# Optimization experiments

Measured on AMD Instinct MI355X. Metric: run time of the kernel, lower is better.

The kernel has to match this reference:

```python
import jax, jax.numpy as jnp
import numpy as np

B, T, H = 64, 512, 256
D = 2 * H            # input dim to slot LSTM (bidirectional encoder repr)
MAX_SLOTS = 64       # max slot spans kept per sentence
MAX_LEN = 8          # max tokens per span
N_SLOT_TYPES = 64


def _pack_spans(bio):
    """Segment BIO tags into spans: each span = B token + following I tokens.
    Returns token index table [B, MAX_SLOTS, MAX_LEN] and validity mask."""
    bsz, t = bio.shape
    bmask = bio == 1
    imask = bio == 2
    sid = jnp.cumsum(bmask.astype(jnp.int32), axis=1) - 1      # span id per token
    valid = (bmask | imask) & (sid >= 0)
    cs = jnp.cumsum(valid.astype(jnp.int32), axis=1)           # running count of span tokens
    bi = jnp.arange(bsz)[:, None]
    # cs value at each span's B token (overflow spans dumped into slot MAX_SLOTS)
    sid_b = jnp.where(bmask & (sid < MAX_SLOTS), sid, MAX_SLOTS)
    start = jnp.zeros((bsz, MAX_SLOTS + 1), jnp.int32).at[bi, sid_b].set(cs)[:, :MAX_SLOTS]
    sid_c = jnp.clip(sid, 0, MAX_SLOTS - 1)
    rank = cs - jnp.take_along_axis(start, sid_c, axis=1)      # position within span (B token -> 0)
    ok = valid & (sid < MAX_SLOTS) & (rank < MAX_LEN)
    s_idx = jnp.where(ok, sid_c, MAX_SLOTS)
    r_idx = jnp.where(ok, rank, MAX_LEN)
    tpos = jnp.broadcast_to(jnp.arange(t, dtype=jnp.int32), (bsz, t))
    tok = jnp.zeros((bsz, MAX_SLOTS + 1, MAX_LEN + 1), jnp.int32).at[bi, s_idx, r_idx].set(tpos)
    vm = jnp.zeros((bsz, MAX_SLOTS + 1, MAX_LEN + 1), bool).at[bi, s_idx, r_idx].set(True)
    return tok[:, :MAX_SLOTS, :MAX_LEN], vm[:, :MAX_SLOTS, :MAX_LEN]


def _lstm(x, Wih, Whh, b):
    """Unidirectional LSTM. x: [N, L, D] -> outputs [N, L, H] (torch gate order i,f,g,o)."""
    xg = jnp.einsum('nld,gd->nlg', x, Wih) + b                 # [N, L, 4H]
    n, l, _ = xg.shape
    h0 = jnp.zeros((n, Whh.shape[1]), x.dtype)

    def step(carry, xt):
        h, c = carry
        g = xt + h @ Whh.T
        i, f, gg, o = jnp.split(g, 4, axis=-1)
        c = jax.nn.sigmoid(f) * c + jax.nn.sigmoid(i) * jnp.tanh(gg)
        h = jax.nn.sigmoid(o) * jnp.tanh(c)
        return (h, c), h

    _, hs = jax.lax.scan(step, (h0, h0), jnp.swapaxes(xg, 0, 1))
    return jnp.swapaxes(hs, 0, 1)


def reference(lstm_repr, W_ih_f, W_hh_f, b_f, W_ih_b, W_hh_b, b_b, slot_emb, bio):
    tok, vm = _pack_spans(bio)                                  # [B,MS,ML], [B,MS,ML]
    bi = jnp.arange(lstm_repr.shape[0])[:, None, None]
    spans = lstm_repr[bi, tok]                                  # [B,MS,ML,D]
    lens = vm.sum(-1)                                           # [B,MS]
    # reverse each span within its valid length (padding stays at the end)
    pos = jnp.arange(MAX_LEN)
    rpos = lens[..., None] - 1 - pos
    ridx = jnp.where(rpos >= 0, rpos, 0)
    spans_rev = jnp.take_along_axis(spans, ridx[..., None], axis=2)
    ms = MAX_SLOTS
    xf = spans.reshape(-1, MAX_LEN, D)
    xb = spans_rev.reshape(-1, MAX_LEN, D)
    m = vm.reshape(-1, MAX_LEN, 1).astype(lstm_repr.dtype)
    hf = _lstm(xf, W_ih_f, W_hh_f, b_f)                         # [B*MS, ML, H]
    hb = _lstm(xb, W_ih_b, W_hh_b, b_b)
    pooled = jnp.concatenate([(hf * m).sum(1), (hb * m).sum(1)], axis=-1)  # sum-pool over span
    pooled = pooled.reshape(lstm_repr.shape[0], ms, 2 * H)
    scores = jnp.einsum('bsh,kh->bsk', pooled, slot_emb)        # [B,MS,n_slot_types]
    scores = scores * (lens > 0)[..., None]
    return scores


def setup_inputs() -> dict:
    key = jax.random.key(0)
    ks = jax.random.split(key, 9)
    s = 0.05
    return {
        'lstm_repr': jax.random.normal(ks[0], (B, T, D), jnp.float32),
        'W_ih_f': jax.random.normal(ks[1], (4 * H, D), jnp.float32) * s,
        'W_hh_f': jax.random.normal(ks[2], (4 * H, H), jnp.float32) * s,
        'b_f': jax.random.normal(ks[3], (4 * H,), jnp.float32) * s,
        'W_ih_b': jax.random.normal(ks[4], (4 * H, D), jnp.float32) * s,
        'W_hh_b': jax.random.normal(ks[5], (4 * H, H), jnp.float32) * s,
        'b_b': jax.random.normal(ks[6], (4 * H,), jnp.float32) * s,
        'slot_emb': jax.random.normal(ks[7], (N_SLOT_TYPES, 2 * H), jnp.float32) * s,
        'bio': jax.random.randint(ks[8], (B, T), 0, 3, dtype=jnp.int32),
    }
```

## Files before the change

### kernel.cpp

```cpp
#include <hip/hip_runtime.h>
#include <hip/hip_bf16.h>
#include <stdint.h>

#define B_ 64
#define T_ 512
#define H_ 256
#define D_ 512
#define MS_ 64
#define ML_ 8
#define NST_ 64

typedef unsigned short u16;
typedef __bf16 bf8 __attribute__((ext_vector_type(8)));
typedef float f4 __attribute__((ext_vector_type(4)));

__device__ __forceinline__ u16 f2bf(float f) {
    unsigned u = __builtin_bit_cast(unsigned, f);
    u += 0x7fffu + ((u >> 16) & 1u);
    return (u16)(u >> 16);
}
__device__ __forceinline__ float bf2f(u16 v) {
    return __builtin_bit_cast(float, (unsigned)v << 16);
}
__device__ __forceinline__ float sigm(float x) { return 1.f / (1.f + __expf(-x)); }

__global__ __launch_bounds__(256) void build_wc2(const float* __restrict__ wihf,
                                                 const float* __restrict__ whhf,
                                                 const float* __restrict__ wihb,
                                                 const float* __restrict__ whhb,
                                                 const float* __restrict__ bf,
                                                 const float* __restrict__ bb,
                                                 u16* __restrict__ wcx,
                                                 u16* __restrict__ wch,
                                                 float* __restrict__ bc) {
    int i = blockIdx.x * 256 + threadIdx.x;
    if (i < 2 * 1024 * 768) {
        int dir = i / (1024 * 768);
        int rem = i - dir * 1024 * 768;
        int n = rem / 768;
        int k = rem - n * 768;
        int nn = n & 63, c = n >> 6;
        int orig = (nn >> 4) * 256 + c * 16 + (nn & 15);
        if (k < 512) {
            const float* wih = dir ? wihb : wihf;
            wcx[((size_t)dir * 1024 + n) * 512 + k] = f2bf(wih[orig * 512 + k]);
        } else {
            const float* whh = dir ? whhb : whhf;
            wch[((size_t)dir * 1024 + n) * 256 + (k - 512)] = f2bf(whh[orig * 256 + (k - 512)]);
        }
    } else if (i < 2 * 1024 * 768 + 2048) {
        int i2 = i - 2 * 1024 * 768;
        int dir = i2 >> 10;
        int n = i2 & 1023;
        int nn = n & 63, c = n >> 6;
        int orig = (nn >> 4) * 256 + c * 16 + (nn & 15);
        bc[i2] = (dir ? bb : bf)[orig];
    }
}

__global__ __launch_bounds__(256) void zero_ws(uint4* __restrict__ dst, int n4) {
    int i = blockIdx.x * 256 + threadIdx.x;
    if (i < n4) { uint4 z = {0u, 0u, 0u, 0u}; dst[i] = z; }
}

__global__ __launch_bounds__(512) void pack_spans2(const int* __restrict__ bio,
                                                   int* __restrict__ tok,
                                                   int* __restrict__ lenb) {
    __shared__ int wsum[8];
    __shared__ int start_s[64];
    __shared__ int len_s[64];
    int b = blockIdx.x;
    int t = threadIdx.x;
    int lane = t & 63, w = t >> 6;
    int v = bio[b * T_ + t];
    int bm = (v == 1);
    int im = (v == 2);
    if (t < 64) len_s[t] = 0;

    int x = bm;
#pragma unroll
    for (int off = 1; off < 64; off <<= 1) {
        int y = __shfl_up(x, off, 64);
        if (lane >= off) x += y;
    }
    if (lane == 63) wsum[w] = x;
    __syncthreads();
    int wof = 0;
    for (int i = 0; i < w; ++i) wof += wsum[i];
    int sid = x + wof - 1;
    int valid = ((bm | im) && sid >= 0) ? 1 : 0;
    __syncthreads();

    x = valid;
#pragma unroll
    for (int off = 1; off < 64; off <<= 1) {
        int y = __shfl_up(x, off, 64);
        if (lane >= off) x += y;
    }
    if (lane == 63) wsum[w] = x;
    __syncthreads();
    wof = 0;
    for (int i = 0; i < w; ++i) wof += wsum[i];
    int cs = x + wof;

    if (bm && sid < MS_) start_s[sid] = cs;
    __syncthreads();

    if (valid && sid < MS_) {
        int rank = cs - start_s[sid];
        if (rank < ML_) {
            tok[(b * MS_ + sid) * ML_ + rank] = t;
            atomicAdd(&len_s[sid], 1);
        }
    }
    __syncthreads();
    if (t < 64) lenb[b * MS_ + t] = len_s[t];
}

__global__ __launch_bounds__(256) void build_lists(const int* __restrict__ lenb,
                                                   int* __restrict__ lists,
                                                   int* __restrict__ counts) {
    __shared__ int wsum[4];
    int tid = threadIdx.x;
    int lane = tid & 63, w = tid >> 6;
    int len[16];
#pragma unroll
    for (int i = 0; i < 16; ++i) len[i] = lenb[tid * 16 + i];
    for (int p = 0; p < ML_; ++p) {
        int c = 0;
#pragma unroll
        for (int i = 0; i < 16; ++i) c += (len[i] > p) ? 1 : 0;
        int x = c;
#pragma unroll
        for (int off = 1; off < 64; off <<= 1) {
            int y = __shfl_up(x, off, 64);
            if (lane >= off) x += y;
        }
        if (lane == 63) wsum[w] = x;
        __syncthreads();
        int wof = 0;
        for (int i = 0; i < w; ++i) wof += wsum[i];
        int pos = wof + x - c;
#pragma unroll
        for (int i = 0; i < 16; ++i)
            if (len[i] > p) lists[p * 4096 + pos++] = tid * 16 + i;
        if (tid == 255) counts[p] = pos;
        __syncthreads();
    }
}

__global__ __launch_bounds__(64) void conv_gather(const float* __restrict__ repr,
                                                  const int* __restrict__ tok,
                                                  const int* __restrict__ lenb,
                                                  u16* __restrict__ xg) {
    int sr = blockIdx.x;
    int span = sr >> 3, rank = sr & 7;
    if (rank >= lenb[span]) return;
    int t = tok[sr];
    int b = span >> 6;
    const float4* src = (const float4*)(repr + (size_t)(b * T_ + t) * D_);
    ushort4* dst = (ushort4*)(xg + (size_t)sr * D_);
    int i = threadIdx.x;
    float4 v0 = src[i * 2], v1 = src[i * 2 + 1];
    ushort4 o0, o1;
    o0.x = f2bf(v0.x); o0.y = f2bf(v0.y); o0.z = f2bf(v0.z); o0.w = f2bf(v0.w);
    o1.x = f2bf(v1.x); o1.y = f2bf(v1.y); o1.z = f2bf(v1.z); o1.w = f2bf(v1.w);
    dst[i * 2] = o0; dst[i * 2 + 1] = o1;
}

__global__ __launch_bounds__(256) void xgate_gemm(const u16* __restrict__ xg,
                                                  const u16* __restrict__ wcx,
                                                  const float* __restrict__ bc,
                                                  const int* __restrict__ lists,
                                                  const int* __restrict__ counts,
                                                  const int* __restrict__ lenb,
                                                  u16* __restrict__ xgates) {
    int gp = blockIdx.y >> 6;
    int dir = gp >> 3, p = gp & 7;
    int rbk = blockIdx.y & 63;
    int cnt = counts[p];
    int base = rbk * 64;
    if (base >= cnt) return;
    int tid = threadIdx.x;

    __shared__ unsigned xoffs[64];
    __shared__ u16 As[64 * 72];
    __shared__ u16 Bs[64 * 72];

    if (tid < 64) {
        unsigned xo = 0;
        int idx = base + tid;
        if (idx < cnt) {
            int span = lists[p * 4096 + idx];
            int L = lenb[span];
            int rank = dir ? (L - 1 - p) : p;
            xo = (unsigned)(span * ML_ + rank) * D_;
        }
        xoffs[tid] = xo;
    }
    __syncthreads();

    int lane = tid & 63;
    int w16 = (tid >> 6) * 16;
    int mr = lane & 15;
    int q = lane >> 4;
    int q8 = q * 8;
    int n0 = blockIdx.x * 64;
    const u16* wb = wcx + (size_t)dir * 1024 * 512;

    f4 acc[4];
    f4 zed = {0.f, 0.f, 0.f, 0.f};
#pragma unroll
    for (int i = 0; i < 4; ++i) acc[i] = zed;

    for (int kt = 0; kt < 8; ++kt) {
#pragma unroll
        for (int i = 0; i < 2; ++i) {
            int c = tid + i * 256;
            int row = c >> 3;
            int cc = (c & 7) * 8;
            *(uint4*)&As[row * 72 + cc] = *(const uint4*)(xg + xoffs[row] + kt * 64 + cc);
            *(uint4*)&Bs[row * 72 + cc] =
                *(const uint4*)(wb + (size_t)(n0 + row) * 512 + kt * 64 + cc);
        }
        __syncthreads();
#pragma unroll
        for (int kk = 0; kk < 64; kk += 32) {
            bf8 af = *(const bf8*)&As[(w16 + mr) * 72 + kk + q8];
#pragma unroll
            for (int nt = 0; nt < 4; ++nt) {
                bf8 bg = *(const bf8*)&Bs[(nt * 16 + mr) * 72 + kk + q8];
                acc[nt] = __builtin_amdgcn_mfma_f32_16x16x32_bf16(af, bg, acc[nt], 0, 0, 0);
            }
        }
        __syncthreads();
    }

    u16 tmp[16];
#pragma unroll
    for (int nt = 0; nt < 4; ++nt)
#pragma unroll
        for (int r = 0; r < 4; ++r) {
            int n = n0 + nt * 16 + mr;
            tmp[nt * 4 + r] = f2bf(acc[nt][r] + bc[dir * 1024 + n]);
        }
    size_t off = ((size_t)blockIdx.y * 16 + blockIdx.x) * 4096 + (size_t)tid * 16;
    *(uint4*)&xgates[off] = *(const uint4*)tmp;
    *(uint4*)&xgates[off + 8] = *(const uint4*)(tmp + 8);
}

__global__ __launch_bounds__(256) void fused_step(const u16* __restrict__ xgates,
                                                  const u16* __restrict__ hin,
                                                  u16* __restrict__ hout,
                                                  const u16* __restrict__ wch,
                                                  const int* __restrict__ lists,
                                                  const int* __restrict__ counts,
                                                  float* __restrict__ cbuf,
                                                  float* __restrict__ pooled, int p) {
    int cnt = counts[p];
    int rb = blockIdx.y;
    int dir = rb >> 6;
    int base = (rb & 63) * 64;
    if (base >= cnt) return;
    int tid = threadIdx.x;

    __shared__ unsigned hoffs[64];
    __shared__ int spans_s[64];
    __shared__ u16 As[64 * 72];
    __shared__ u16 Bs[64 * 72];

    if (tid < 64) {
        int span = 0;
        int idx = base + tid;
        if (idx < cnt) span = lists[p * 4096 + idx];
        spans_s[tid] = span;
        hoffs[tid] = (unsigned)(dir * 4096 + span) * H_;
    }
    __syncthreads();

    int lane = tid & 63;
    int w16 = (tid >> 6) * 16;
    int mr = lane & 15;
    int q = lane >> 4;
    int q8 = q * 8;
    int n0 = blockIdx.x * 64;
    const u16* wb = wch + (size_t)dir * 1024 * 256;

    int gp = dir * 8 + p;
    size_t xoff = ((size_t)(gp * 64 + (rb & 63)) * 16 + blockIdx.x) * 4096 + (size_t)tid * 16;
    u16 tmp[16];
    *(uint4*)tmp = *(const uint4*)(xgates + xoff);
    *(uint4*)(tmp + 8) = *(const uint4*)(xgates + xoff + 8);
    f4 acc[4];
#pragma unroll
    for (int nt = 0; nt < 4; ++nt)
#pragma unroll
        for (int r = 0; r < 4; ++r) acc[nt][r] = bf2f(tmp[nt * 4 + r]);

    for (int kt = 0; kt < 4; ++kt) {
#pragma unroll
        for (int i = 0; i < 2; ++i) {
            int c = tid + i * 256;
            int row = c >> 3;
            int cc = (c & 7) * 8;
            *(uint4*)&As[row * 72 + cc] = *(const uint4*)(hin + hoffs[row] + kt * 64 + cc);
            *(uint4*)&Bs[row * 72 + cc] =
                *(const uint4*)(wb + (size_t)(n0 + row) * 256 + kt * 64 + cc);
        }
        __syncthreads();
#pragma unroll
        for (int kk = 0; kk < 64; kk += 32) {
            bf8 af = *(const bf8*)&As[(w16 + mr) * 72 + kk + q8];
#pragma unroll
            for (int nt = 0; nt < 4; ++nt) {
                bf8 bg = *(const bf8*)&Bs[(nt * 16 + mr) * 72 + kk + q8];
                acc[nt] = __builtin_amdgcn_mfma_f32_16x16x32_bf16(af, bg, acc[nt], 0, 0, 0);
            }
        }
        __syncthreads();
    }

    int j = blockIdx.x * 16 + mr;
#pragma unroll
    for (int r = 0; r < 4; ++r) {
        int m = w16 + q * 4 + r;
        if (base + m < cnt) {
            int span = spans_s[m];
            float gi = acc[0][r], gf = acc[1][r], gg = acc[2][r], go = acc[3][r];
            int si = (dir * 4096 + span) * H_ + j;
            float c = cbuf[si];
            float cn = sigm(gf) * c + sigm(gi) * tanhf(gg);
            float h = sigm(go) * tanhf(cn);
            cbuf[si] = cn;
            hout[si] = f2bf(h);
            pooled[span * 512 + dir * H_ + j] += h;
        }
    }
}

__global__ __launch_bounds__(256) void scores_mfma(const float* __restrict__ pooled,
                                                   const float* __restrict__ emb,
                                                   float* __restrict__ out) {
    int g = blockIdx.x;
    int tid = threadIdx.x;

    __shared__ u16 As[64 * 72];
    __shared__ u16 Bs[64 * 72];

    int lane = tid & 63;
    int w16 = (tid >> 6) * 16;
    int mr = lane & 15;
    int q = lane >> 4;
    int q8 = q * 8;

    f4 acc[4];
    f4 zed = {0.f, 0.f, 0.f, 0.f};
#pragma unroll
    for (int i = 0; i < 4; ++i) acc[i] = zed;

    for (int kt = 0; kt < 8; ++kt) {
#pragma unroll
        for (int i = 0; i < 2; ++i) {
            int c = tid + i * 256;
            int row = c >> 3;
            int cc = (c & 7) * 8;
            const float4* a = (const float4*)(pooled + (size_t)(g * 64 + row) * 512 + kt * 64 + cc);
            float4 v0 = a[0], v1 = a[1];
            ushort4 o0, o1;
            o0.x = f2bf(v0.x); o0.y = f2bf(v0.y); o0.z = f2bf(v0.z); o0.w = f2bf(v0.w);
            o1.x = f2bf(v1.x); o1.y = f2bf(v1.y); o1.z = f2bf(v1.z); o1.w = f2bf(v1.w);
            *(ushort4*)&As[row * 72 + cc] = o0;
            *(ushort4*)&As[row * 72 + cc + 4] = o1;
            const float4* b = (const float4*)(emb + (size_t)row * 512 + kt * 64 + cc);
            float4 w0 = b[0], w1 = b[1];
            ushort4 p0, p1;
            p0.x = f2bf(w0.x); p0.y = f2bf(w0.y); p0.z = f2bf(w0.z); p0.w = f2bf(w0.w);
            p1.x = f2bf(w1.x); p1.y = f2bf(w1.y); p1.z = f2bf(w1.z); p1.w = f2bf(w1.w);
            *(ushort4*)&Bs[row * 72 + cc] = p0;
            *(ushort4*)&Bs[row * 72 + cc + 4] = p1;
        }
        __syncthreads();
#pragma unroll
        for (int kk = 0; kk < 64; kk += 32) {
            bf8 af = *(const bf8*)&As[(w16 + mr) * 72 + kk + q8];
#pragma unroll
            for (int nt = 0; nt < 4; ++nt) {
                bf8 bg = *(const bf8*)&Bs[(nt * 16 + mr) * 72 + kk + q8];
                acc[nt] = __builtin_amdgcn_mfma_f32_16x16x32_bf16(af, bg, acc[nt], 0, 0, 0);
            }
        }
        __syncthreads();
    }

#pragma unroll
    for (int nt = 0; nt < 4; ++nt) {
#pragma unroll
        for (int r = 0; r < 4; ++r) {
            int m = g * 64 + w16 + q * 4 + r;
            int n = nt * 16 + mr;
            out[(size_t)m * 64 + n] = acc[nt][r];
        }
    }
}


extern "C" void kernel_launch(void* const* d_in, const int* in_sizes, int n_in,
                              void* d_out, int out_size, void* d_ws, size_t ws_size,
                              hipStream_t stream) {
    const float* lstm_repr = (const float*)d_in[0];
    const float* W_ih_f = (const float*)d_in[1];
    const float* W_hh_f = (const float*)d_in[2];
    const float* b_f    = (const float*)d_in[3];
    const float* W_ih_b = (const float*)d_in[4];
    const float* W_hh_b = (const float*)d_in[5];
    const float* b_b    = (const float*)d_in[6];
    const float* slot_emb = (const float*)d_in[7];
    const int* bio      = (const int*)d_in[8];
    float* out = (float*)d_out;

    char* ws = (char*)d_ws;
    u16*  xg     = (u16*)(ws + 0);
    u16*  xgates = (u16*)(ws + 33554432);
    u16*  wcx    = (u16*)(ws + 167772160);
    u16*  wch    = (u16*)(ws + 169869312);
    float* bc    = (float*)(ws + 170917888);
    int*  tok    = (int*)(ws + 170926080);
    int*  lenb   = (int*)(ws + 171057152);
    int*  lists  = (int*)(ws + 171073536);
    int*  counts = (int*)(ws + 171204608);
    float* pooled= (float*)(ws + 171204864);
    float* cbuf  = (float*)(ws + 179593472);
    u16*  hbf    = (u16*)(ws + 187982080);
    u16* hb[2] = { hbf, hbf + 2 * 4096 * 256 };

    build_wc2<<<6152, 256, 0, stream>>>(W_ih_f, W_hh_f, W_ih_b, W_hh_b, b_f, b_b,
                                        wcx, wch, bc);
    zero_ws<<<6144, 256, 0, stream>>>((uint4*)pooled, 1572864);
    pack_spans2<<<64, 512, 0, stream>>>(bio, tok, lenb);
    build_lists<<<1, 256, 0, stream>>>(lenb, lists, counts);
    conv_gather<<<32768, 64, 0, stream>>>(lstm_repr, tok, lenb, xg);

    xgate_gemm<<<dim3(16, 1024), 256, 0, stream>>>(xg, wcx, bc, lists, counts, lenb,
                                                   xgates);

    for (int p = 0; p < 8; ++p) {
        fused_step<<<dim3(16, 128), 256, 0, stream>>>(xgates, hb[p & 1], hb[1 - (p & 1)],
                                                      wch, lists, counts, cbuf, pooled, p);
    }
    scores_mfma<<<64, 256, 0, stream>>>(pooled, slot_emb, out);
}
```

Baseline: 298.4 us.

## Widen GEMM tiles to 256 columns, special-case first LSTM step, drop zeroing

The x-gate GEMM and the recurrent step kernels now compute four 64-column tiles per block, so each A tile is loaded once and reused across 256 output columns instead of 64. Block indices are linearised and swizzled. The first timestep gets its own pointwise-only kernel, because h and c start at zero and no recurrent GEMM is needed. That kernel writes pooled directly, which removes the workspace zeroing pass, and the scores kernel now masks rows with empty spans explicitly. The gather kernel packs four rows per block. The trade-off is 64 accumulator vectors per thread and four times the LDS per block, which may lower occupancy.

```diff
diff --git a/kernel.cpp b/kernel.cpp
--- a/kernel.cpp
+++ b/kernel.cpp
@@ -58,11 +58,6 @@
     }
 }
 
-__global__ __launch_bounds__(256) void zero_ws(uint4* __restrict__ dst, int n4) {
-    int i = blockIdx.x * 256 + threadIdx.x;
-    if (i < n4) { uint4 z = {0u, 0u, 0u, 0u}; dst[i] = z; }
-}
-
 __global__ __launch_bounds__(512) void pack_spans2(const int* __restrict__ bio,
                                                    int* __restrict__ tok,
                                                    int* __restrict__ lenb) {
@@ -149,18 +144,19 @@
     }
 }
 
-__global__ __launch_bounds__(64) void conv_gather(const float* __restrict__ repr,
-                                                  const int* __restrict__ tok,
-                                                  const int* __restrict__ lenb,
-                                                  u16* __restrict__ xg) {
-    int sr = blockIdx.x;
+__global__ __launch_bounds__(256) void conv_gather(const float* __restrict__ repr,
+                                                   const int* __restrict__ tok,
+                                                   const int* __restrict__ lenb,
+                                                   u16* __restrict__ xg) {
+    int tid = threadIdx.x;
+    int sr = blockIdx.x * 4 + (tid >> 6);
+    int i = tid & 63;
     int span = sr >> 3, rank = sr & 7;
     if (rank >= lenb[span]) return;
     int t = tok[sr];
     int b = span >> 6;
     const float4* src = (const float4*)(repr + (size_t)(b * T_ + t) * D_);
     ushort4* dst = (ushort4*)(xg + (size_t)sr * D_);
-    int i = threadIdx.x;
     float4 v0 = src[i * 2], v1 = src[i * 2 + 1];
     ushort4 o0, o1;
     o0.x = f2bf(v0.x); o0.y = f2bf(v0.y); o0.z = f2bf(v0.z); o0.w = f2bf(v0.w);
@@ -168,16 +164,20 @@
     dst[i * 2] = o0; dst[i * 2 + 1] = o1;
 }
 
-__global__ __launch_bounds__(256) void xgate_gemm(const u16* __restrict__ xg,
-                                                  const u16* __restrict__ wcx,
-                                                  const float* __restrict__ bc,
-                                                  const int* __restrict__ lists,
-                                                  const int* __restrict__ counts,
-                                                  const int* __restrict__ lenb,
-                                                  u16* __restrict__ xgates) {
-    int gp = blockIdx.y >> 6;
+__global__ __launch_bounds__(256) void xgate_gemm4(const u16* __restrict__ xg,
+                                                   const u16* __restrict__ wcx,
+                                                   const float* __restrict__ bc,
+                                                   const int* __restrict__ lists,
+                                                   const int* __restrict__ counts,
+                                                   const int* __restrict__ lenb,
+                                                   u16* __restrict__ xgates) {
+    int lin = blockIdx.x;
+    int rr = lin & 7;
+    int xs = (lin >> 3) & 3;
+    int y  = (lin >> 5) * 8 + rr;
+    int gp = y >> 6;
     int dir = gp >> 3, p = gp & 7;
-    int rbk = blockIdx.y & 63;
+    int rbk = y & 63;
     int cnt = counts[p];
     int base = rbk * 64;
     if (base >= cnt) return;
@@ -185,7 +185,7 @@
 
     __shared__ unsigned xoffs[64];
     __shared__ u16 As[64 * 72];
-    __shared__ u16 Bs[64 * 72];
+    __shared__ u16 Bs[4 * 64 * 72];
 
     if (tid < 64) {
         unsigned xo = 0;
@@ -205,13 +205,13 @@
     int mr = lane & 15;
     int q = lane >> 4;
     int q8 = q * 8;
-    int n0 = blockIdx.x * 64;
+    int n0 = xs * 256;
     const u16* wb = wcx + (size_t)dir * 1024 * 512;
 
-    f4 acc[4];
+    f4 acc[16];
     f4 zed = {0.f, 0.f, 0.f, 0.f};
 #pragma unroll
-    for (int i = 0; i < 4; ++i) acc[i] = zed;
+    for (int i = 0; i < 16; ++i) acc[i] = zed;
 
     for (int kt = 0; kt < 8; ++kt) {
 #pragma unroll
@@ -220,54 +220,132 @@
             int row = c >> 3;
             int cc = (c & 7) * 8;
             *(uint4*)&As[row * 72 + cc] = *(const uint4*)(xg + xoffs[row] + kt * 64 + cc);
-            *(uint4*)&Bs[row * 72 + cc] =
-                *(const uint4*)(wb + (size_t)(n0 + row) * 512 + kt * 64 + cc);
+        }
+#pragma unroll
+        for (int i = 0; i < 8; ++i) {
+            int c2 = tid + i * 256;
+            int ntile = c2 >> 9;
+            int rem = c2 & 511;
+            int row = rem >> 3;
+            int cc = (rem & 7) * 8;
+            *(uint4*)&Bs[ntile * 4608 + row * 72 + cc] =
+                *(const uint4*)(wb + (size_t)(n0 + ntile * 64 + row) * 512 + kt * 64 + cc);
         }
         __syncthreads();
 #pragma unroll
         for (int kk = 0; kk < 64; kk += 32) {
             bf8 af = *(const bf8*)&As[(w16 + mr) * 72 + kk + q8];
 #pragma unroll
-            for (int nt = 0; nt < 4; ++nt) {
-                bf8 bg = *(const bf8*)&Bs[(nt * 16 + mr) * 72 + kk + q8];
-                acc[nt] = __builtin_amdgcn_mfma_f32_16x16x32_bf16(af, bg, acc[nt], 0, 0, 0);
+            for (int ntile = 0; ntile < 4; ++ntile) {
+#pragma unroll
+                for (int nt = 0; nt < 4; ++nt) {
+                    bf8 bg = *(const bf8*)&Bs[ntile * 4608 + (nt * 16 + mr) * 72 + kk + q8];
+                    acc[ntile * 4 + nt] =
+                        __builtin_amdgcn_mfma_f32_16x16x32_bf16(af, bg, acc[ntile * 4 + nt], 0, 0, 0);
+                }
             }
         }
         __syncthreads();
     }
 
-    u16 tmp[16];
-#pragma unroll
-    for (int nt = 0; nt < 4; ++nt)
+    u16 tmp[64];
+#pragma unroll
+    for (int ntile = 0; ntile < 4; ++ntile)
+#pragma unroll
+        for (int nt = 0; nt < 4; ++nt)
+#pragma unroll
+            for (int r = 0; r < 4; ++r) {
+                int n = n0 + ntile * 64 + nt * 16 + mr;
+                tmp[ntile * 16 + nt * 4 + r] = f2bf(acc[ntile * 4 + nt][r] + bc[dir * 1024 + n]);
+            }
+    size_t off = ((size_t)(y * 4 + xs) * 256 + tid) * 64;
+    uint4* dst = (uint4*)(xgates + off);
+#pragma unroll
+    for (int i = 0; i < 8; ++i) dst[i] = ((const uint4*)tmp)[i];
+}
+
+__global__ __launch_bounds__(256) void point0(const u16* __restrict__ xgates,
+                                              const int* __restrict__ lists,
+                                              const int* __restrict__ counts,
+                                              float* __restrict__ cbuf,
+                                              u16* __restrict__ hout,
+                                              float* __restrict__ pooled) {
+    int dir = blockIdx.x >> 6;
+    int rbk = blockIdx.x & 63;
+    int cnt = counts[0];
+    int base = rbk * 64;
+    if (base >= cnt) return;
+    int tid = threadIdx.x;
+
+    __shared__ int spans_s[64];
+    if (tid < 64) {
+        int span = 0;
+        int idx = base + tid;
+        if (idx < cnt) span = lists[idx];
+        spans_s[tid] = span;
+    }
+    __syncthreads();
+
+    int lane = tid & 63;
+    int w16 = (tid >> 6) * 16;
+    int mr = lane & 15;
+    int q = lane >> 4;
+    int y = dir * 512 + rbk;
+
+#pragma unroll
+    for (int xs = 0; xs < 4; ++xs) {
+        u16 tmp[64];
+        const uint4* s = (const uint4*)(xgates + ((size_t)(y * 4 + xs) * 256 + tid) * 64);
+#pragma unroll
+        for (int i = 0; i < 8; ++i) ((uint4*)tmp)[i] = s[i];
 #pragma unroll
         for (int r = 0; r < 4; ++r) {
-            int n = n0 + nt * 16 + mr;
-            tmp[nt * 4 + r] = f2bf(acc[nt][r] + bc[dir * 1024 + n]);
-        }
-    size_t off = ((size_t)blockIdx.y * 16 + blockIdx.x) * 4096 + (size_t)tid * 16;
-    *(uint4*)&xgates[off] = *(const uint4*)tmp;
-    *(uint4*)&xgates[off + 8] = *(const uint4*)(tmp + 8);
-}
-
-__global__ __launch_bounds__(256) void fused_step(const u16* __restrict__ xgates,
-                                                  const u16* __restrict__ hin,
-                                                  u16* __restrict__ hout,
-                                                  const u16* __restrict__ wch,
-                                                  const int* __restrict__ lists,
-                                                  const int* __restrict__ counts,
-                                                  float* __restrict__ cbuf,
-                                                  float* __restrict__ pooled, int p) {
+            int m = w16 + q * 4 + r;
+            if (base + m < cnt) {
+                int span = spans_s[m];
+#pragma unroll
+                for (int ntile = 0; ntile < 4; ++ntile) {
+                    int j = (xs * 4 + ntile) * 16 + mr;
+                    float gi = bf2f(tmp[ntile * 16 + 0 + r]);
+                    float gf = bf2f(tmp[ntile * 16 + 4 + r]);
+                    float gg = bf2f(tmp[ntile * 16 + 8 + r]);
+                    float go = bf2f(tmp[ntile * 16 + 12 + r]);
+                    (void)gf;
+                    float cn = sigm(gi) * tanhf(gg);
+                    float h = sigm(go) * tanhf(cn);
+                    int si = (dir * 4096 + span) * H_ + j;
+                    cbuf[si] = cn;
+                    hout[si] = f2bf(h);
+                    pooled[span * 512 + dir * H_ + j] = h;
+                }
+            }
+        }
+    }
+}
+
+__global__ __launch_bounds__(256) void fused_step4(const u16* __restrict__ xgates,
+                                                   const u16* __restrict__ hin,
+                                                   u16* __restrict__ hout,
+                                                   const u16* __restrict__ wch,
+                                                   const int* __restrict__ lists,
+                                                   const int* __restrict__ counts,
+                                                   float* __restrict__ cbuf,
+                                                   float* __restrict__ pooled, int p) {
+    int lin = blockIdx.x;
+    int rr = lin & 7;
+    int xs = (lin >> 3) & 3;
+    int yb = (lin >> 5) * 8 + rr;
+    int dir = yb >> 6;
+    int rbk = yb & 63;
     int cnt = counts[p];
-    int rb = blockIdx.y;
-    int dir = rb >> 6;
-    int base = (rb & 63) * 64;
+    int base = rbk * 64;
     if (base >= cnt) return;
     int tid = threadIdx.x;
 
     __shared__ unsigned hoffs[64];
     __shared__ int spans_s[64];
     __shared__ u16 As[64 * 72];
-    __shared__ u16 Bs[64 * 72];
+    __shared__ u16 Bs[4 * 64 * 72];
 
     if (tid < 64) {
         int span = 0;
@@ -283,19 +361,25 @@
     int mr = lane & 15;
     int q = lane >> 4;
     int q8 = q * 8;
-    int n0 = blockIdx.x * 64;
+    int n0 = xs * 256;
     const u16* wb = wch + (size_t)dir * 1024 * 256;
 
     int gp = dir * 8 + p;
-    size_t xoff = ((size_t)(gp * 64 + (rb & 63)) * 16 + blockIdx.x) * 4096 + (size_t)tid * 16;
-    u16 tmp[16];
-    *(uint4*)tmp = *(const uint4*)(xgates + xoff);
-    *(uint4*)(tmp + 8) = *(const uint4*)(xgates + xoff + 8);
-    f4 acc[4];
-#pragma unroll
-    for (int nt = 0; nt < 4; ++nt)
-#pragma unroll
-        for (int r = 0; r < 4; ++r) acc[nt][r] = bf2f(tmp[nt * 4 + r]);
+    int y = gp * 64 + rbk;
+    u16 tmp[64];
+    {
+        const uint4* s = (const uint4*)(xgates + ((size_t)(y * 4 + xs) * 256 + tid) * 64);
+#pragma unroll
+        for (int i = 0; i < 8; ++i) ((uint4*)tmp)[i] = s[i];
+    }
+    f4 acc[16];
+#pragma unroll
+    for (int ntile = 0; ntile < 4; ++ntile)
+#pragma unroll
+        for (int nt = 0; nt < 4; ++nt)
+#pragma unroll
+            for (int r = 0; r < 4; ++r)
+                acc[ntile * 4 + nt][r] = bf2f(tmp[ntile * 16 + nt * 4 + r]);
 
     for (int kt = 0; kt < 4; ++kt) {
 #pragma unroll
@@ -304,42 +388,61 @@
             int row = c >> 3;
             int cc = (c & 7) * 8;
             *(uint4*)&As[row * 72 + cc] = *(const uint4*)(hin + hoffs[row] + kt * 64 + cc);
-            *(uint4*)&Bs[row * 72 + cc] =
-                *(const uint4*)(wb + (size_t)(n0 + row) * 256 + kt * 64 + cc);
+        }
+#pragma unroll
+        for (int i = 0; i < 8; ++i) {
+            int c2 = tid + i * 256;
+            int ntile = c2 >> 9;
+            int rem = c2 & 511;
+            int row = rem >> 3;
+            int cc = (rem & 7) * 8;
+            *(uint4*)&Bs[ntile * 4608 + row * 72 + cc] =
+                *(const uint4*)(wb + (size_t)(n0 + ntile * 64 + row) * 256 + kt * 64 + cc);
         }
         __syncthreads();
 #pragma unroll
         for (int kk = 0; kk < 64; kk += 32) {
             bf8 af = *(const bf8*)&As[(w16 + mr) * 72 + kk + q8];
 #pragma unroll
-            for (int nt = 0; nt < 4; ++nt) {
-                bf8 bg = *(const bf8*)&Bs[(nt * 16 + mr) * 72 + kk + q8];
-                acc[nt] = __builtin_amdgcn_mfma_f32_16x16x32_bf16(af, bg, acc[nt], 0, 0, 0);
+            for (int ntile = 0; ntile < 4; ++ntile) {
+#pragma unroll
+                for (int nt = 0; nt < 4; ++nt) {
+                    bf8 bg = *(const bf8*)&Bs[ntile * 4608 + (nt * 16 + mr) * 72 + kk + q8];
+                    acc[ntile * 4 + nt] =
+                        __builtin_amdgcn_mfma_f32_16x16x32_bf16(af, bg, acc[ntile * 4 + nt], 0, 0, 0);
+                }
             }
         }
         __syncthreads();
     }
 
-    int j = blockIdx.x * 16 + mr;
 #pragma unroll
     for (int r = 0; r < 4; ++r) {
         int m = w16 + q * 4 + r;
         if (base + m < cnt) {
             int span = spans_s[m];
-            float gi = acc[0][r], gf = acc[1][r], gg = acc[2][r], go = acc[3][r];
-            int si = (dir * 4096 + span) * H_ + j;
-            float c = cbuf[si];
-            float cn = sigm(gf) * c + sigm(gi) * tanhf(gg);
-            float h = sigm(go) * tanhf(cn);
-            cbuf[si] = cn;
-            hout[si] = f2bf(h);
-            pooled[span * 512 + dir * H_ + j] += h;
+#pragma unroll
+            for (int ntile = 0; ntile < 4; ++ntile) {
+                int j = (xs * 4 + ntile) * 16 + mr;
+                float gi = acc[ntile * 4 + 0][r];
+                float gf = acc[ntile * 4 + 1][r];
+                float gg = acc[ntile * 4 + 2][r];
+                float go = acc[ntile * 4 + 3][r];
+                int si = (dir * 4096 + span) * H_ + j;
+                float c = cbuf[si];
+                float cn = sigm(gf) * c + sigm(gi) * tanhf(gg);
+                float h = sigm(go) * tanhf(cn);
+                cbuf[si] = cn;
+                hout[si] = f2bf(h);
+                pooled[span * 512 + dir * H_ + j] += h;
+            }
         }
     }
 }
 
 __global__ __launch_bounds__(256) void scores_mfma(const float* __restrict__ pooled,
                                                    const float* __restrict__ emb,
+                                                   const int* __restrict__ lenb,
                                                    float* __restrict__ out) {
     int g = blockIdx.x;
     int tid = threadIdx.x;
@@ -393,12 +496,13 @@
     }
 
 #pragma unroll
-    for (int nt = 0; nt < 4; ++nt) {
-#pragma unroll
-        for (int r = 0; r < 4; ++r) {
-            int m = g * 64 + w16 + q * 4 + r;
+    for (int r = 0; r < 4; ++r) {
+        int m = g * 64 + w16 + q * 4 + r;
+        int ln = lenb[m];
+#pragma unroll
+        for (int nt = 0; nt < 4; ++nt) {
             int n = nt * 16 + mr;
-            out[(size_t)m * 64 + n] = acc[nt][r];
+            out[(size_t)m * 64 + n] = (ln > 0) ? acc[nt][r] : 0.f;
         }
     }
 }
@@ -435,17 +539,17 @@
 
     build_wc2<<<6152, 256, 0, stream>>>(W_ih_f, W_hh_f, W_ih_b, W_hh_b, b_f, b_b,
                                         wcx, wch, bc);
-    zero_ws<<<6144, 256, 0, stream>>>((uint4*)pooled, 1572864);
     pack_spans2<<<64, 512, 0, stream>>>(bio, tok, lenb);
     build_lists<<<1, 256, 0, stream>>>(lenb, lists, counts);
-    conv_gather<<<32768, 64, 0, stream>>>(lstm_repr, tok, lenb, xg);
-
-    xgate_gemm<<<dim3(16, 1024), 256, 0, stream>>>(xg, wcx, bc, lists, counts, lenb,
-                                                   xgates);
-
-    for (int p = 0; p < 8; ++p) {
-        fused_step<<<dim3(16, 128), 256, 0, stream>>>(xgates, hb[p & 1], hb[1 - (p & 1)],
-                                                      wch, lists, counts, cbuf, pooled, p);
-    }
-    scores_mfma<<<64, 256, 0, stream>>>(pooled, slot_emb, out);
-}
+    conv_gather<<<8192, 256, 0, stream>>>(lstm_repr, tok, lenb, xg);
+
+    xgate_gemm4<<<4096, 256, 0, stream>>>(xg, wcx, bc, lists, counts, lenb, xgates);
+
+    point0<<<128, 256, 0, stream>>>(xgates, lists, counts, cbuf, hb[1], pooled);
+
+    for (int p = 1; p < 8; ++p) {
+        fused_step4<<<512, 256, 0, stream>>>(xgates, hb[p & 1], hb[1 - (p & 1)],
+                                             wch, lists, counts, cbuf, pooled, p);
+    }
+    scores_mfma<<<64, 256, 0, stream>>>(pooled, slot_emb, lenb, out);
+}
```

Measured after the change: 374.9 us. 1.26x slower.
